# Kernel optimization log

Hardware: AMD Instinct MI355X
Metric: run time of the kernel (lower is better)

## Reference

```python
import jax, jax.numpy as jnp
import numpy as np

HEADS = 20          # 1280 / 64 head_dim, standard SD UNet attention
LORA_SCALE = 1.0    # lora_scale init arg


def setup_inputs() -> dict:
    key = jax.random.key(0)
    ks = jax.random.split(key, 16)
    def w(k, shape, s=0.02):
        return jax.random.normal(k, shape, dtype=jnp.float32) * s
    H, C, R = 1280, 768, 64  # hidden_size, cross_attention_dim, lora_rank
    return {
        "hidden_states": jax.random.normal(ks[0], (16, 4096, H), dtype=jnp.float32),
        "encoder_hidden_states": jax.random.normal(ks[1], (16, 77, C), dtype=jnp.float32),
        # base attention projections (diffusers: q/k/v no bias, to_out has bias)
        "Wq": w(ks[2], (H, H)), "Wk": w(ks[3], (C, H)), "Wv": w(ks[4], (C, H)),
        "Wo": w(ks[5], (H, H)), "bo": jnp.zeros((H,), dtype=jnp.float32),
        # LoRA adapters (down: in->rank, up: rank->out, no bias)
        "q_down": w(ks[6], (H, R)), "q_up": w(ks[7], (R, H)),
        "k_down": w(ks[8], (C, R)), "k_up": w(ks[9], (R, H)),
        "v_down": w(ks[10], (C, R)), "v_up": w(ks[11], (R, H)),
        "o_down": w(ks[12], (H, R)), "o_up": w(ks[13], (R, H)),
    }


def reference(hidden_states, encoder_hidden_states, Wq, Wk, Wv, Wo, bo,
              q_down, q_up, k_down, k_up, v_down, v_up, o_down, o_up):
    b, sq, _ = hidden_states.shape
    # base projections + LoRA low-rank corrections
    q = hidden_states @ Wq + LORA_SCALE * ((hidden_states @ q_down) @ q_up)
    k = encoder_hidden_states @ Wk + LORA_SCALE * ((encoder_hidden_states @ k_down) @ k_up)
    v = encoder_hidden_states @ Wv + LORA_SCALE * ((encoder_hidden_states @ v_down) @ v_up)

    d = q.shape[-1] // HEADS
    def split_heads(x):  # [b, s, h*d] -> [b, h, s, d]
        return x.reshape(x.shape[0], x.shape[1], HEADS, d).transpose(0, 2, 1, 3)
    qh, kh, vh = split_heads(q), split_heads(k), split_heads(v)

    # scaled dot-product attention (no mask, non-causal, dropout=0)
    scale = 1.0 / np.sqrt(d).astype(np.float32)
    scores = jnp.einsum('bhqd,bhkd->bhqk', qh, kh) * scale
    probs = jax.nn.softmax(scores, axis=-1)
    attn_out = jnp.einsum('bhqk,bhkd->bhqd', probs, vh)
    attn_out = attn_out.transpose(0, 2, 1, 3).reshape(b, sq, HEADS * d)

    # output projection + LoRA on W_O
    out = attn_out @ Wo + bo + LORA_SCALE * ((attn_out @ o_down) @ o_up)
    return out
```

## Files before the change

### kernel.cpp

```cpp
#include <hip/hip_runtime.h>
#include <hip/hip_bf16.h>
#include <stdint.h>

typedef unsigned short u16;
typedef __attribute__((ext_vector_type(8))) short short8;
typedef __attribute__((ext_vector_type(4))) float f32x4;

__device__ __forceinline__ u16 f2bf(float f) {
  union { float f; unsigned u; } v; v.f = f;
  unsigned r = v.u + 0x7fffu + ((v.u >> 16) & 1u);
  return (u16)(r >> 16);
}

__device__ __forceinline__ void g2lds16(const u16* g, u16* l) {
  __builtin_amdgcn_global_load_lds(
      (const __attribute__((address_space(1))) uint32_t*)g,
      (__attribute__((address_space(3))) uint32_t*)l, 16, 0, 0);
}

#define BAR()   asm volatile("s_barrier" ::: "memory")
#define LGKM0() asm volatile("s_waitcnt lgkmcnt(0)" ::: "memory")
#define VM8()   asm volatile("s_waitcnt vmcnt(8)" ::: "memory")
#define VM6()   asm volatile("s_waitcnt vmcnt(6)" ::: "memory")
#define VM0()   asm volatile("s_waitcnt vmcnt(0)" ::: "memory")
#define PRIO1() __builtin_amdgcn_s_setprio(1)
#define PRIO0() __builtin_amdgcn_s_setprio(0)

#define QSCALE 0.18033688f

__global__ __launch_bounds__(256) void k_prepc(
    const float* __restrict__ hs, u16* __restrict__ hs_b,
    const float* __restrict__ ehs, u16* __restrict__ ehs_b,
    const float* __restrict__ Wq, const float* __restrict__ qd, const float* __restrict__ qu, u16* __restrict__ wq_t,
    const float* __restrict__ Wk, const float* __restrict__ kd, const float* __restrict__ ku, u16* __restrict__ wk_t,
    const float* __restrict__ Wv, const float* __restrict__ vd, const float* __restrict__ vu, u16* __restrict__ wv_t,
    const float* __restrict__ Wo, const float* __restrict__ od, const float* __restrict__ ou, u16* __restrict__ wo_t) {
  __shared__ float dn[64][65];
  __shared__ float up[64][17];
  int bid = blockIdx.x;

  if (bid < 40960) {
    int i = bid * 256 + threadIdx.x;
    const float4* p = (const float4*)(hs + (size_t)i * 8);
    float4 a = p[0], b = p[1];
    short8 o;
    o[0] = (short)f2bf(a.x); o[1] = (short)f2bf(a.y);
    o[2] = (short)f2bf(a.z); o[3] = (short)f2bf(a.w);
    o[4] = (short)f2bf(b.x); o[5] = (short)f2bf(b.y);
    o[6] = (short)f2bf(b.z); o[7] = (short)f2bf(b.w);
    *(short8*)(hs_b + (size_t)i * 8) = o;
    return;
  }
  bid -= 40960;
  if (bid < 480) {
    int i = bid * 256 + threadIdx.x;
    short8 o;
    if (i < 118272) {
      const float4* p = (const float4*)(ehs + (size_t)i * 8);
      float4 a = p[0], b = p[1];
      o[0] = (short)f2bf(a.x); o[1] = (short)f2bf(a.y);
      o[2] = (short)f2bf(a.z); o[3] = (short)f2bf(a.w);
      o[4] = (short)f2bf(b.x); o[5] = (short)f2bf(b.y);
      o[6] = (short)f2bf(b.z); o[7] = (short)f2bf(b.w);
    } else {
#pragma unroll
      for (int e = 0; e < 8; ++e) o[e] = 0;
    }
    *(short8*)(ehs_b + (size_t)i * 8) = o;
    return;
  }
  bid -= 480;
  const float *W, *dng, *upg; u16* Wt; int K, bx, by;
  if (bid < 1600)      { W = Wq; dng = qd; upg = qu; Wt = wq_t; K = 1280; bx = bid % 20; by = bid / 20; }
  else if (bid < 2560) { bid -= 1600; W = Wk; dng = kd; upg = ku; Wt = wk_t; K = 768;  bx = bid % 12; by = bid / 12; }
  else if (bid < 3520) { bid -= 2560; W = Wv; dng = vd; upg = vu; Wt = wv_t; K = 768;  bx = bid % 12; by = bid / 12; }
  else                 { bid -= 3520; W = Wo; dng = od; upg = ou; Wt = wo_t; K = 1280; bx = bid % 20; by = bid / 20; }
  const int N = 1280;
  const int k0 = bx * 64, n0 = by * 16;
  const int kc = threadIdx.x & 63, ty = threadIdx.x >> 6;
  for (int c = threadIdx.x; c < 4096; c += 256)
    dn[c >> 6][c & 63] = dng[(size_t)(k0 + (c >> 6)) * 64 + (c & 63)];
  for (int c = threadIdx.x; c < 1024; c += 256)
    up[c >> 4][c & 15] = upg[(size_t)(c >> 4) * N + n0 + (c & 15)];
  __syncthreads();
  float acc[4];
#pragma unroll
  for (int e = 0; e < 4; ++e)
    acc[e] = W[(size_t)(k0 + kc) * N + n0 + ty * 4 + e];
#pragma unroll 16
  for (int r = 0; r < 64; ++r) {
    float d = dn[kc][r];
#pragma unroll
    for (int e = 0; e < 4; ++e) acc[e] += d * up[r][ty * 4 + e];
  }
#pragma unroll
  for (int e = 0; e < 4; ++e)
    Wt[(size_t)(n0 + ty * 4 + e) * K + k0 + kc] = f2bf(acc[e]);
}

__global__ __launch_bounds__(256) void k_gemmKV(const u16* __restrict__ A,
                                                const u16* __restrict__ BtK,
                                                const u16* __restrict__ BtV,
                                                u16* __restrict__ CK,
                                                u16* __restrict__ CV) {
  constexpr int N = 1280, K = 768;
  const u16* Bt = blockIdx.z ? BtV : BtK;
  u16* Cout = blockIdx.z ? CV : CK;
  __shared__ __align__(16) u16 As[128 * 32];
  __shared__ __align__(16) u16 Bs[128 * 32];
  const int tid = threadIdx.x, lane = tid & 63, w = tid >> 6;
  const int n0 = blockIdx.x * 128, m0 = blockIdx.y * 128;
  const int wm = (w >> 1) * 64, wn = (w & 1) * 64;

  f32x4 acc[4][4];
  f32x4 zf = {0.f, 0.f, 0.f, 0.f};
#pragma unroll
  for (int i = 0; i < 4; ++i)
#pragma unroll
    for (int j = 0; j < 4; ++j) acc[i][j] = zf;

  const int c0 = w, c1 = w + 4;
  const int rA0 = c0 * 16 + (lane >> 2), rA1 = c1 * 16 + (lane >> 2);
  const int kp = (lane & 3) * 8;
  const u16* gA0 = A + (size_t)(m0 + rA0) * K + kp;
  const u16* gA1 = A + (size_t)(m0 + rA1) * K + kp;
  const u16* gB0 = Bt + (size_t)(n0 + rA0) * K + kp;
  const u16* gB1 = Bt + (size_t)(n0 + rA1) * K + kp;
  u16* lA0 = As + c0 * 512;  u16* lA1 = As + c1 * 512;
  u16* lB0 = Bs + c0 * 512;  u16* lB1 = Bs + c1 * 512;

  const int fr = lane & 15, kg = (lane >> 4) * 8;

  for (int k0 = 0; k0 < K; k0 += 32) {
    g2lds16(gA0 + k0, lA0);
    g2lds16(gA1 + k0, lA1);
    g2lds16(gB0 + k0, lB0);
    g2lds16(gB1 + k0, lB1);
    __syncthreads();
    short8 af[4], bf[4];
#pragma unroll
    for (int i = 0; i < 4; ++i)
      af[i] = *(const short8*)(As + (wm + i * 16 + fr) * 32 + kg);
#pragma unroll
    for (int j = 0; j < 4; ++j)
      bf[j] = *(const short8*)(Bs + (wn + j * 16 + fr) * 32 + kg);
#pragma unroll
    for (int i = 0; i < 4; ++i)
#pragma unroll
      for (int j = 0; j < 4; ++j)
        acc[i][j] = __builtin_amdgcn_mfma_f32_16x16x32_bf16(af[i], bf[j], acc[i][j], 0, 0, 0);
    __syncthreads();
  }

  const int rb = (lane >> 4) * 4;
#pragma unroll
  for (int i = 0; i < 4; ++i)
#pragma unroll
    for (int j = 0; j < 4; ++j) {
      int col = n0 + wn + j * 16 + fr;
#pragma unroll
      for (int r = 0; r < 4; ++r) {
        int row = m0 + wm + i * 16 + rb + r;
        Cout[(size_t)row * N + col] = f2bf(acc[i][j][r]);
      }
    }
}

#define GEMM256_COMMON()                                                       \
  constexpr int K = 1280;                                                      \
  constexpr int N = 1280;                                                      \
  __shared__ __align__(16) u16 lds[2][2][2][128 * 64];                         \
  const int lane = threadIdx.x & 63, w = threadIdx.x >> 6;                     \
  const int bid = blockIdx.x;                                                  \
  const int tile = (bid & 7) * 160 + (bid >> 3);                               \
  const int n0 = (tile % 5) * 256, m0 = (tile / 5) * 256;                      \
  const int l0 = w * 2;                                                        \
  const int fr = lane & 15;                                                    \
  const int q16b = (lane >> 4) * 16;                                           \
  const int xr = (fr & 7) << 4;                                                \
  const int cT0 = ((0 + q16b) ^ xr) >> 1;                                      \
  const int cT1 = ((64 + q16b) ^ xr) >> 1;                                     \
  const int ha = w >> 2;                                                       \
  const int hb = (w & 3) >> 1;                                                 \
  const int rB0 = (w & 1) * 64;

#define GSRC_INIT(A_, Bt_)                                                     \
  const u16* gsrc[4][2];                                                       \
  _Pragma("unroll") for (int s2 = 0; s2 < 4; ++s2) {                           \
    const int side = s2 >> 1, h = s2 & 1;                                      \
    _Pragma("unroll") for (int l = 0; l < 2; ++l) {                            \
      const int o = (l0 + l) * 1024 + lane * 16;                               \
      const int row = o >> 7;                                                  \
      const int scol = (o & 127) ^ ((row & 7) << 4);                           \
      const u16* base = side ? ((Bt_) + (size_t)(n0 + h * 128 + row) * K)      \
                             : ((A_) + (size_t)(m0 + h * 128 + row) * K);      \
      gsrc[s2][l] = base + (scol >> 1);                                        \
    }                                                                          \
  }

#define STAGE_HALF(P, SIDE, H, KT)                                             \
  do {                                                                         \
    g2lds16(gsrc[(SIDE) * 2 + (H)][0] + (KT) * 64,                             \
            &lds[P][SIDE][H][(l0 + 0) * 512]);                                 \
    g2lds16(gsrc[(SIDE) * 2 + (H)][1] + (KT) * 64,                             \
            &lds[P][SIDE][H][(l0 + 1) * 512]);                                 \
  } while (0)

#define STAGE_FULL(P, KT)                                                      \
  do {                                                                         \
    STAGE_HALF(P, 0, 0, KT); STAGE_HALF(P, 0, 1, KT);                          \
    STAGE_HALF(P, 1, 0, KT); STAGE_HALF(P, 1, 1, KT);                          \
  } while (0)

#define LOAD_AF(P, IB)                                                         \
  do {                                                                         \
    _Pragma("unroll") for (int ii = 0; ii < 4; ++ii) {                         \
      const u16* rp = &lds[P][0][ha][(((IB) + ii) * 16 + fr) * 64];            \
      af[ii][0] = *(const short8*)(rp + cT0);                                  \
      af[ii][1] = *(const short8*)(rp + cT1);                                  \
    }                                                                          \
  } while (0)

#define LOAD_BF(P, JB)                                                         \
  do {                                                                         \
    _Pragma("unroll") for (int jj = 0; jj < 2; ++jj) {                         \
      const u16* rp = &lds[P][1][hb][(rB0 + ((JB) + jj) * 16 + fr) * 64];      \
      bf[(JB) + jj][0] = *(const short8*)(rp + cT0);                           \
      bf[(JB) + jj][1] = *(const short8*)(rp + cT1);                           \
    }                                                                          \
  } while (0)

#define MFMA_Q(IO, JB)                                                         \
  do {                                                                         \
    _Pragma("unroll") for (int t = 0; t < 2; ++t)                              \
        _Pragma("unroll") for (int ii = 0; ii < 4; ++ii)                       \
            _Pragma("unroll") for (int jj = 0; jj < 2; ++jj)                   \
                acc[(IO) + ii][(JB) + jj] =                                    \
        __builtin_amdgcn_mfma_f32_16x16x32_bf16(                               \
            af[ii][t], bf[(JB) + jj][t], acc[(IO) + ii][(JB) + jj], 0, 0, 0);  \
  } while (0)

#define ACC_ZERO()                                                             \
  do {                                                                         \
    f32x4 zf = {0.f, 0.f, 0.f, 0.f};                                           \
    _Pragma("unroll") for (int i = 0; i < 8; ++i)                              \
        _Pragma("unroll") for (int j = 0; j < 4; ++j) acc[i][j] = zf;          \
  } while (0)

#define GEMM256_EPI_F32BIAS()                                                  \
  do {                                                                         \
    float* C = (float*)Cout;                                                   \
    _Pragma("unroll") for (int i = 0; i < 8; ++i)                              \
        _Pragma("unroll") for (int j = 0; j < 4; ++j) {                        \
      const int col = ocol + j * 16 + fr;                                      \
      const float bj = bias[col];                                              \
      _Pragma("unroll") for (int r = 0; r < 4; ++r)                            \
          C[(size_t)(orow + i * 16 + rb + r) * N + col] = acc[i][j][r] + bj;   \
    }                                                                          \
  } while (0)

#define GEMM256_EPI_BF16SCALE()                                                \
  do {                                                                         \
    u16* C = (u16*)Cout;                                                       \
    _Pragma("unroll") for (int i = 0; i < 8; ++i)                              \
        _Pragma("unroll") for (int j = 0; j < 4; ++j) {                        \
      const int col = ocol + j * 16 + fr;                                      \
      _Pragma("unroll") for (int r = 0; r < 4; ++r)                            \
          C[(size_t)(orow + i * 16 + rb + r) * N + col] =                      \
              f2bf(acc[i][j][r] * QSCALE);                                     \
    }                                                                          \
  } while (0)

template <int OUT_MODE>
__global__ __launch_bounds__(512, 2) void k_gemm256f(const u16* __restrict__ A,
                                                     const u16* __restrict__ Bt,
                                                     void* __restrict__ Cout,
                                                     const float* __restrict__ bias) {
  GEMM256_COMMON();
  GSRC_INIT(A, Bt);

  short8 af[4][2], bf[4][2];
  f32x4 acc[8][4];
  ACC_ZERO();

  STAGE_FULL(0, 0);
  STAGE_FULL(1, 1);
  VM8();
  BAR();

  for (int t = 0; t < 20; ++t) {
    const int P = t & 1;
    LOAD_AF(P, 0);
    LOAD_BF(P, 0);
    LOAD_BF(P, 2);
    MFMA_Q(0, 0);
    MFMA_Q(0, 2);
    LOAD_AF(P, 4);
    MFMA_Q(4, 2);
    LGKM0();
    BAR();
    if (t < 18) STAGE_FULL(P, t + 2);
    PRIO1(); MFMA_Q(4, 0); PRIO0();
    if (t < 18) { VM8(); } else { VM0(); }
    BAR();
  }

  const int rb = (lane >> 4) * 4;
  const int orow = m0 + (w >> 2) * 128;
  const int ocol = n0 + (w & 3) * 64;
  if (OUT_MODE == 1) { GEMM256_EPI_F32BIAS(); }
  else               { GEMM256_EPI_BF16SCALE(); }
}

__global__ __launch_bounds__(512, 2) void k_gemm256p(const u16* __restrict__ A,
                                                     const u16* __restrict__ Bt,
                                                     void* __restrict__ Cout) {
  GEMM256_COMMON();
  GSRC_INIT(A, Bt);

  short8 af[4][2], bf[4][2];
  f32x4 acc[8][4];
  ACC_ZERO();

  STAGE_FULL(0, 0);
  STAGE_FULL(1, 1);
  VM8();
  BAR();

  for (int it = 0; it < 10; ++it) {
    const bool st = (it < 9);
    const int t2 = 2 * it + 2, t3 = 2 * it + 3;
    LOAD_AF(0, 0); LOAD_BF(0, 0);
    BAR(); LGKM0(); PRIO1(); MFMA_Q(0, 0); PRIO0(); BAR();
    LOAD_BF(0, 2);
    BAR(); LGKM0(); PRIO1(); MFMA_Q(0, 2); PRIO0(); BAR();
    LOAD_AF(0, 4);
    if (st) STAGE_HALF(0, 1, 0, t2);
    BAR(); LGKM0(); PRIO1(); MFMA_Q(4, 2); PRIO0(); BAR();
    if (st) { STAGE_HALF(0, 1, 1, t2); STAGE_HALF(0, 0, 0, t2); }
    PRIO1(); MFMA_Q(4, 0); PRIO0();
    if (st) { VM6(); } else { VM0(); }
    BAR();
    LOAD_AF(1, 0); LOAD_BF(1, 0);
    if (st) STAGE_HALF(0, 0, 1, t2);
    BAR(); LGKM0(); PRIO1(); MFMA_Q(0, 0); PRIO0(); BAR();
    LOAD_BF(1, 2);
    BAR(); LGKM0(); PRIO1(); MFMA_Q(0, 2); PRIO0(); BAR();
    LOAD_AF(1, 4);
    if (st) STAGE_HALF(1, 1, 0, t3);
    BAR(); LGKM0(); PRIO1(); MFMA_Q(4, 2); PRIO0(); BAR();
    if (st) { STAGE_HALF(1, 1, 1, t3); STAGE_HALF(1, 0, 0, t3); STAGE_HALF(1, 0, 1, t3); }
    PRIO1(); MFMA_Q(4, 0); PRIO0();
    if (st) { VM8(); } else { VM0(); }
    BAR();
  }

  const int rb = (lane >> 4) * 4;
  const int orow = m0 + (w >> 2) * 128;
  const int ocol = n0 + (w & 3) * 64;
  GEMM256_EPI_BF16SCALE();
}

__global__ __launch_bounds__(256) void k_attn(u16* __restrict__ Q,
                                              const u16* __restrict__ Kb,
                                              const u16* __restrict__ Vb) {
  const int mt = blockIdx.x, h = blockIdx.y, b = blockIdx.z;
  const int tid = threadIdx.x, lane = tid & 63, w = tid >> 6;
  const int m0 = b * 4096 + mt * 128;
  const int ccol = h * 64;

  __shared__ __align__(16) u16 Qs[128 * 64];
  __shared__ __align__(16) u16 Kl[80 * 72];
  __shared__ __align__(16) u16 Vt[64 * 104];
  __shared__ __align__(16) u16 Pl[128 * 104];

#pragma unroll
  for (int c = 0; c < 4; ++c) {
    const int o = (c * 4 + w) * 1024 + lane * 16;
    const int row = o >> 7;
    const int scol = (o & 127) ^ ((row & 7) << 4);
    g2lds16(Q + (size_t)(m0 + row) * 1280 + ccol + (scol >> 1),
            Qs + (size_t)(c * 4 + w) * 512);
  }

  {
    short8 zz;
#pragma unroll
    for (int e = 0; e < 8; ++e) zz[e] = 0;
    if (tid < 27) ((short8*)Kl)[693 + tid] = zz;
    { const int prow = tid >> 1, pc0 = 80 + (tid & 1) * 8;
      *(short8*)(Pl + prow * 104 + pc0) = zz; }
    for (int c = tid; c < 2048; c += 256)
      Vt[(c >> 5) * 104 + 64 + (c & 31)] = 0;
  }
  for (int c = tid; c < 616; c += 256) {
    int s = c >> 3, d0 = (c & 7) * 8;
    short8 v = *(const short8*)(Kb + (size_t)(b * 77 + s) * 1280 + ccol + d0);
    *(short8*)(Kl + s * 72 + d0) = v;
  }
  for (int c = tid; c < 616; c += 256) {
    int s = c >> 3, d0 = (c & 7) * 8;
    short8 v = *(const short8*)(Vb + (size_t)(b * 77 + s) * 1280 + ccol + d0);
#pragma unroll
    for (int e = 0; e < 8; ++e) Vt[(d0 + e) * 104 + s] = (u16)v[e];
  }
  __syncthreads();

  const int cb = lane & 15;
  const int kq = lane >> 4;
  const int kgu = kq * 8;

  short8 qf[2][2];
#pragma unroll
  for (int i = 0; i < 2; ++i)
#pragma unroll
    for (int t2 = 0; t2 < 2; ++t2) {
      const int r_ = w * 32 + i * 16 + cb;
      const int bc = (t2 * 64 + kq * 16) ^ ((r_ & 7) << 4);
      qf[i][t2] = *(const short8*)(Qs + r_ * 64 + (bc >> 1));
    }

  f32x4 sc[2][5];
  {
    f32x4 zf = {0.f, 0.f, 0.f, 0.f};
#pragma unroll
    for (int i = 0; i < 2; ++i)
#pragma unroll
      for (int j = 0; j < 5; ++j) sc[i][j] = zf;
  }
#pragma unroll
  for (int t2 = 0; t2 < 2; ++t2) {
    short8 kf[5];
#pragma unroll
    for (int j = 0; j < 5; ++j)
      kf[j] = *(const short8*)(Kl + (j * 16 + cb) * 72 + t2 * 32 + kgu);
#pragma unroll
    for (int i = 0; i < 2; ++i)
#pragma unroll
      for (int j = 0; j < 5; ++j)
        sc[i][j] = __builtin_amdgcn_mfma_f32_16x16x32_bf16(qf[i][t2], kf[j], sc[i][j], 0, 0, 0);
  }

  float inv[2][4];
#pragma unroll
  for (int i = 0; i < 2; ++i) {
#pragma unroll
    for (int r = 0; r < 4; ++r) {
      float sum = 0.f;
#pragma unroll
      for (int j = 0; j < 4; ++j) {
        float pv = exp2f(sc[i][j][r]);
        sc[i][j][r] = pv;
        sum += pv;
      }
      {
        float pv = (cb < 13) ? exp2f(sc[i][4][r]) : 0.f;
        sc[i][4][r] = pv;
        sum += pv;
      }
#pragma unroll
      for (int mk = 8; mk >= 1; mk >>= 1) sum += __shfl_xor(sum, mk, 64);
      inv[i][r] = 1.f / sum;
    }
  }

  {
    const int rbase = kq * 4;
#pragma unroll
    for (int i = 0; i < 2; ++i)
#pragma unroll
      for (int j = 0; j < 5; ++j)
#pragma unroll
        for (int r = 0; r < 4; ++r)
          Pl[(w * 32 + i * 16 + rbase + r) * 104 + j * 16 + cb] = f2bf(sc[i][j][r]);
  }
  __syncthreads();

  f32x4 o[2][4];
  {
    f32x4 zf = {0.f, 0.f, 0.f, 0.f};
#pragma unroll
    for (int i = 0; i < 2; ++i)
#pragma unroll
      for (int n = 0; n < 4; ++n) o[i][n] = zf;
  }
#pragma unroll
  for (int t2 = 0; t2 < 3; ++t2) {
    short8 pf[2], vf[4];
#pragma unroll
    for (int i = 0; i < 2; ++i)
      pf[i] = *(const short8*)(Pl + (w * 32 + i * 16 + cb) * 104 + t2 * 32 + kgu);
#pragma unroll
    for (int n = 0; n < 4; ++n)
      vf[n] = *(const short8*)(Vt + (n * 16 + cb) * 104 + t2 * 32 + kgu);
#pragma unroll
    for (int i = 0; i < 2; ++i)
#pragma unroll
      for (int n = 0; n < 4; ++n)
        o[i][n] = __builtin_amdgcn_mfma_f32_16x16x32_bf16(pf[i], vf[n], o[i][n], 0, 0, 0);
  }

  {
    const int rbase = kq * 4;
#pragma unroll
    for (int i = 0; i < 2; ++i)
#pragma unroll
      for (int n = 0; n < 4; ++n)
#pragma unroll
        for (int r = 0; r < 4; ++r)
          Pl[(w * 32 + i * 16 + rbase + r) * 104 + n * 16 + cb] =
              f2bf(o[i][n][r] * inv[i][r]);
  }
  __syncthreads();

#pragma unroll
  for (int c2 = 0; c2 < 4; ++c2) {
    const int o2 = (c2 * 256 + tid) * 16;
    const int row = o2 >> 7, bc = (o2 & 127) >> 1;
    short8 v = *(const short8*)(Pl + row * 104 + bc);
    *(short8*)(Q + (size_t)(m0 + row) * 1280 + ccol + bc) = v;
  }
}

extern "C" void kernel_launch(void* const* d_in, const int* in_sizes, int n_in,
                              void* d_out, int out_size, void* d_ws, size_t ws_size,
                              hipStream_t stream) {
  (void)in_sizes; (void)n_in; (void)out_size; (void)ws_size;
  const float* hs  = (const float*)d_in[0];
  const float* ehs = (const float*)d_in[1];
  const float* Wq  = (const float*)d_in[2];
  const float* Wk  = (const float*)d_in[3];
  const float* Wv  = (const float*)d_in[4];
  const float* Wo  = (const float*)d_in[5];
  const float* bo  = (const float*)d_in[6];
  const float* qd  = (const float*)d_in[7];
  const float* qu  = (const float*)d_in[8];
  const float* kd  = (const float*)d_in[9];
  const float* ku  = (const float*)d_in[10];
  const float* vd  = (const float*)d_in[11];
  const float* vu  = (const float*)d_in[12];
  const float* od  = (const float*)d_in[13];
  const float* ou  = (const float*)d_in[14];

  char* p = (char*)d_ws;
  u16* q_buf = (u16*)p;  p += (size_t)65536 * 1280 * 2;
  u16* wq_t  = (u16*)p;  p += (size_t)1280 * 1280 * 2;
  u16* wo_t  = (u16*)p;  p += (size_t)1280 * 1280 * 2;
  u16* wk_t  = (u16*)p;  p += (size_t)1280 * 768 * 2;
  u16* wv_t  = (u16*)p;  p += (size_t)1280 * 768 * 2;
  u16* ehs_b = (u16*)p;  p += (size_t)1280 * 768 * 2;
  u16* k_buf = (u16*)p;  p += (size_t)1280 * 1280 * 2;
  u16* v_buf = (u16*)p;  p += (size_t)1280 * 1280 * 2;
  u16* hs_b  = (u16*)d_out;

  k_prepc<<<46560, 256, 0, stream>>>(hs, hs_b, ehs, ehs_b,
                                     Wq, qd, qu, wq_t,
                                     Wk, kd, ku, wk_t,
                                     Wv, vd, vu, wv_t,
                                     Wo, od, ou, wo_t);

  k_gemm256p<<<1280, 512, 0, stream>>>(hs_b, wq_t, q_buf);
  k_gemmKV<<<dim3(10, 10, 2), 256, 0, stream>>>(ehs_b, wk_t, wv_t, k_buf, v_buf);

  k_attn<<<dim3(32, 20, 16), 256, 0, stream>>>(q_buf, k_buf, v_buf);

  k_gemm256f<1><<<1280, 512, 0, stream>>>(q_buf, wo_t, d_out, bo);
}
```

Measured before the change: 726.1 us.

## Fuse attention into Q-projection GEMM epilogue with pre-transposed V

Removes the separate attention kernel and computes attention directly in the Q-projection GEMM epilogue. Each wave of a 256x256 tile owns one 64-wide head, loads that head's K and V fragments straight from global memory into registers, and runs softmax(QK)V over 32-row chunks using LDS scratch. The KV GEMM now writes V already transposed per head, padded to 96 keys and zero-filled in the prep kernel, so no LDS transpose is needed. This drops the write and re-read of the Q buffer and one kernel launch. In exchange it runs at one block per CU instead of two and replaces the previous hand-scheduled Q GEMM main loop with the simpler shared one.

Result: faster. 704.7 us, median of 2 (-2.9%).

```diff
diff --git a/kernel.cpp b/kernel.cpp
--- a/kernel.cpp
+++ b/kernel.cpp
@@ -21,7 +21,6 @@
 #define BAR()   asm volatile("s_barrier" ::: "memory")
 #define LGKM0() asm volatile("s_waitcnt lgkmcnt(0)" ::: "memory")
 #define VM8()   asm volatile("s_waitcnt vmcnt(8)" ::: "memory")
-#define VM6()   asm volatile("s_waitcnt vmcnt(6)" ::: "memory")
 #define VM0()   asm volatile("s_waitcnt vmcnt(0)" ::: "memory")
 #define PRIO1() __builtin_amdgcn_s_setprio(1)
 #define PRIO0() __builtin_amdgcn_s_setprio(0)
@@ -31,6 +30,7 @@
 __global__ __launch_bounds__(256) void k_prepc(
     const float* __restrict__ hs, u16* __restrict__ hs_b,
     const float* __restrict__ ehs, u16* __restrict__ ehs_b,
+    u16* __restrict__ vt,
     const float* __restrict__ Wq, const float* __restrict__ qd, const float* __restrict__ qu, u16* __restrict__ wq_t,
     const float* __restrict__ Wk, const float* __restrict__ kd, const float* __restrict__ ku, u16* __restrict__ wk_t,
     const float* __restrict__ Wv, const float* __restrict__ vd, const float* __restrict__ vu, u16* __restrict__ wv_t,
@@ -70,6 +70,15 @@
     return;
   }
   bid -= 480;
+  if (bid < 960) {
+    int i = bid * 256 + threadIdx.x;
+    short8 z;
+#pragma unroll
+    for (int e = 0; e < 8; ++e) z[e] = 0;
+    *(short8*)(vt + (size_t)i * 8) = z;
+    return;
+  }
+  bid -= 960;
   const float *W, *dng, *upg; u16* Wt; int K, bx, by;
   if (bid < 1600)      { W = Wq; dng = qd; upg = qu; Wt = wq_t; K = 1280; bx = bid % 20; by = bid / 20; }
   else if (bid < 2560) { bid -= 1600; W = Wk; dng = kd; upg = ku; Wt = wk_t; K = 768;  bx = bid % 12; by = bid / 12; }
@@ -102,10 +111,9 @@
                                                 const u16* __restrict__ BtK,
                                                 const u16* __restrict__ BtV,
                                                 u16* __restrict__ CK,
-                                                u16* __restrict__ CV) {
+                                                u16* __restrict__ VT) {
   constexpr int N = 1280, K = 768;
   const u16* Bt = blockIdx.z ? BtV : BtK;
-  u16* Cout = blockIdx.z ? CV : CK;
   __shared__ __align__(16) u16 As[128 * 32];
   __shared__ __align__(16) u16 Bs[128 * 32];
   const int tid = threadIdx.x, lane = tid & 63, w = tid >> 6;
@@ -153,17 +161,36 @@
   }
 
   const int rb = (lane >> 4) * 4;
-#pragma unroll
-  for (int i = 0; i < 4; ++i)
-#pragma unroll
-    for (int j = 0; j < 4; ++j) {
-      int col = n0 + wn + j * 16 + fr;
-#pragma unroll
-      for (int r = 0; r < 4; ++r) {
-        int row = m0 + wm + i * 16 + rb + r;
-        Cout[(size_t)row * N + col] = f2bf(acc[i][j][r]);
+  if (blockIdx.z == 0) {
+#pragma unroll
+    for (int i = 0; i < 4; ++i)
+#pragma unroll
+      for (int j = 0; j < 4; ++j) {
+        int col = n0 + wn + j * 16 + fr;
+#pragma unroll
+        for (int r = 0; r < 4; ++r) {
+          int row = m0 + wm + i * 16 + rb + r;
+          CK[(size_t)row * N + col] = f2bf(acc[i][j][r]);
+        }
       }
-    }
+  } else {
+#pragma unroll
+    for (int i = 0; i < 4; ++i)
+#pragma unroll
+      for (int j = 0; j < 4; ++j) {
+        int col = n0 + wn + j * 16 + fr;
+        int h = col >> 6, d = col & 63;
+#pragma unroll
+        for (int r = 0; r < 4; ++r) {
+          int row = m0 + wm + i * 16 + rb + r;
+          if (row < 1232) {
+            int b2 = row / 77;
+            int s2 = row - b2 * 77;
+            VT[(size_t)((b2 * 20 + h) * 64 + d) * 96 + s2] = f2bf(acc[i][j][r]);
+          }
+        }
+      }
+  }
 }
 
 #define GEMM256_COMMON()                                                       \
@@ -247,278 +274,203 @@
         _Pragma("unroll") for (int j = 0; j < 4; ++j) acc[i][j] = zf;          \
   } while (0)
 
-#define GEMM256_EPI_F32BIAS()                                                  \
-  do {                                                                         \
-    float* C = (float*)Cout;                                                   \
-    _Pragma("unroll") for (int i = 0; i < 8; ++i)                              \
-        _Pragma("unroll") for (int j = 0; j < 4; ++j) {                        \
-      const int col = ocol + j * 16 + fr;                                      \
-      const float bj = bias[col];                                              \
-      _Pragma("unroll") for (int r = 0; r < 4; ++r)                            \
-          C[(size_t)(orow + i * 16 + rb + r) * N + col] = acc[i][j][r] + bj;   \
+#define GEMM256_MAINLOOP()                                                     \
+  do {                                                                         \
+    STAGE_FULL(0, 0);                                                          \
+    STAGE_FULL(1, 1);                                                          \
+    VM8();                                                                     \
+    BAR();                                                                     \
+    for (int t = 0; t < 20; ++t) {                                             \
+      const int P = t & 1;                                                     \
+      LOAD_AF(P, 0);                                                           \
+      LOAD_BF(P, 0);                                                           \
+      LOAD_BF(P, 2);                                                           \
+      MFMA_Q(0, 0);                                                            \
+      MFMA_Q(0, 2);                                                            \
+      LOAD_AF(P, 4);                                                           \
+      MFMA_Q(4, 2);                                                            \
+      LGKM0();                                                                 \
+      BAR();                                                                   \
+      if (t < 18) STAGE_FULL(P, t + 2);                                        \
+      PRIO1(); MFMA_Q(4, 0); PRIO0();                                          \
+      if (t < 18) { VM8(); } else { VM0(); }                                   \
+      BAR();                                                                   \
     }                                                                          \
   } while (0)
 
-#define GEMM256_EPI_BF16SCALE()                                                \
-  do {                                                                         \
-    u16* C = (u16*)Cout;                                                       \
-    _Pragma("unroll") for (int i = 0; i < 8; ++i)                              \
-        _Pragma("unroll") for (int j = 0; j < 4; ++j) {                        \
-      const int col = ocol + j * 16 + fr;                                      \
-      _Pragma("unroll") for (int r = 0; r < 4; ++r)                            \
-          C[(size_t)(orow + i * 16 + rb + r) * N + col] =                      \
-              f2bf(acc[i][j][r] * QSCALE);                                     \
-    }                                                                          \
-  } while (0)
-
-template <int OUT_MODE>
 __global__ __launch_bounds__(512, 2) void k_gemm256f(const u16* __restrict__ A,
                                                      const u16* __restrict__ Bt,
-                                                     void* __restrict__ Cout,
+                                                     float* __restrict__ Cout,
                                                      const float* __restrict__ bias) {
   GEMM256_COMMON();
   GSRC_INIT(A, Bt);
-
   short8 af[4][2], bf[4][2];
   f32x4 acc[8][4];
   ACC_ZERO();
-
-  STAGE_FULL(0, 0);
-  STAGE_FULL(1, 1);
-  VM8();
-  BAR();
-
-  for (int t = 0; t < 20; ++t) {
-    const int P = t & 1;
-    LOAD_AF(P, 0);
-    LOAD_BF(P, 0);
-    LOAD_BF(P, 2);
-    MFMA_Q(0, 0);
-    MFMA_Q(0, 2);
-    LOAD_AF(P, 4);
-    MFMA_Q(4, 2);
-    LGKM0();
-    BAR();
-    if (t < 18) STAGE_FULL(P, t + 2);
-    PRIO1(); MFMA_Q(4, 0); PRIO0();
-    if (t < 18) { VM8(); } else { VM0(); }
-    BAR();
-  }
+  GEMM256_MAINLOOP();
 
   const int rb = (lane >> 4) * 4;
   const int orow = m0 + (w >> 2) * 128;
   const int ocol = n0 + (w & 3) * 64;
-  if (OUT_MODE == 1) { GEMM256_EPI_F32BIAS(); }
-  else               { GEMM256_EPI_BF16SCALE(); }
-}
-
-__global__ __launch_bounds__(512, 2) void k_gemm256p(const u16* __restrict__ A,
-                                                     const u16* __restrict__ Bt,
-                                                     void* __restrict__ Cout) {
+#pragma unroll
+  for (int i = 0; i < 8; ++i)
+#pragma unroll
+    for (int j = 0; j < 4; ++j) {
+      const int col = ocol + j * 16 + fr;
+      const float bj = bias[col];
+#pragma unroll
+      for (int r = 0; r < 4; ++r)
+        Cout[(size_t)(orow + i * 16 + rb + r) * N + col] = acc[i][j][r] + bj;
+    }
+}
+
+__global__ __launch_bounds__(512, 1) void k_gemm256qa(const u16* __restrict__ A,
+                                                      const u16* __restrict__ Bt,
+                                                      const u16* __restrict__ Kbuf,
+                                                      const u16* __restrict__ VTg,
+                                                      u16* __restrict__ Obuf) {
   GEMM256_COMMON();
   GSRC_INIT(A, Bt);
-
   short8 af[4][2], bf[4][2];
   f32x4 acc[8][4];
   ACC_ZERO();
-
-  STAGE_FULL(0, 0);
-  STAGE_FULL(1, 1);
-  VM8();
-  BAR();
-
-  for (int it = 0; it < 10; ++it) {
-    const bool st = (it < 9);
-    const int t2 = 2 * it + 2, t3 = 2 * it + 3;
-    LOAD_AF(0, 0); LOAD_BF(0, 0);
-    BAR(); LGKM0(); PRIO1(); MFMA_Q(0, 0); PRIO0(); BAR();
-    LOAD_BF(0, 2);
-    BAR(); LGKM0(); PRIO1(); MFMA_Q(0, 2); PRIO0(); BAR();
-    LOAD_AF(0, 4);
-    if (st) STAGE_HALF(0, 1, 0, t2);
-    BAR(); LGKM0(); PRIO1(); MFMA_Q(4, 2); PRIO0(); BAR();
-    if (st) { STAGE_HALF(0, 1, 1, t2); STAGE_HALF(0, 0, 0, t2); }
-    PRIO1(); MFMA_Q(4, 0); PRIO0();
-    if (st) { VM6(); } else { VM0(); }
-    BAR();
-    LOAD_AF(1, 0); LOAD_BF(1, 0);
-    if (st) STAGE_HALF(0, 0, 1, t2);
-    BAR(); LGKM0(); PRIO1(); MFMA_Q(0, 0); PRIO0(); BAR();
-    LOAD_BF(1, 2);
-    BAR(); LGKM0(); PRIO1(); MFMA_Q(0, 2); PRIO0(); BAR();
-    LOAD_AF(1, 4);
-    if (st) STAGE_HALF(1, 1, 0, t3);
-    BAR(); LGKM0(); PRIO1(); MFMA_Q(4, 2); PRIO0(); BAR();
-    if (st) { STAGE_HALF(1, 1, 1, t3); STAGE_HALF(1, 0, 0, t3); STAGE_HALF(1, 0, 1, t3); }
-    PRIO1(); MFMA_Q(4, 0); PRIO0();
-    if (st) { VM8(); } else { VM0(); }
-    BAR();
-  }
-
-  const int rb = (lane >> 4) * 4;
+  GEMM256_MAINLOOP();
+
+  const int bb = (tile / 5) >> 4;
+  const int hd = (tile % 5) * 4 + (w & 3);
   const int orow = m0 + (w >> 2) * 128;
-  const int ocol = n0 + (w & 3) * 64;
-  GEMM256_EPI_BF16SCALE();
-}
-
-__global__ __launch_bounds__(256) void k_attn(u16* __restrict__ Q,
-                                              const u16* __restrict__ Kb,
-                                              const u16* __restrict__ Vb) {
-  const int mt = blockIdx.x, h = blockIdx.y, b = blockIdx.z;
-  const int tid = threadIdx.x, lane = tid & 63, w = tid >> 6;
-  const int m0 = b * 4096 + mt * 128;
-  const int ccol = h * 64;
-
-  __shared__ __align__(16) u16 Qs[128 * 64];
-  __shared__ __align__(16) u16 Kl[80 * 72];
-  __shared__ __align__(16) u16 Vt[64 * 104];
-  __shared__ __align__(16) u16 Pl[128 * 104];
-
-#pragma unroll
-  for (int c = 0; c < 4; ++c) {
-    const int o = (c * 4 + w) * 1024 + lane * 16;
-    const int row = o >> 7;
-    const int scol = (o & 127) ^ ((row & 7) << 4);
-    g2lds16(Q + (size_t)(m0 + row) * 1280 + ccol + (scol >> 1),
-            Qs + (size_t)(c * 4 + w) * 512);
-  }
+  const int cb = fr, kq = lane >> 4, kgu = kq * 8;
+
+  u16* ldsb = (u16*)lds;
+  u16* Qc = ldsb + w * 2304;
+  u16* Pw = ldsb + 8 * 2304 + w * 3328;
 
   {
     short8 zz;
 #pragma unroll
     for (int e = 0; e < 8; ++e) zz[e] = 0;
-    if (tid < 27) ((short8*)Kl)[693 + tid] = zz;
-    { const int prow = tid >> 1, pc0 = 80 + (tid & 1) * 8;
-      *(short8*)(Pl + prow * 104 + pc0) = zz; }
-    for (int c = tid; c < 2048; c += 256)
-      Vt[(c >> 5) * 104 + 64 + (c & 31)] = 0;
-  }
-  for (int c = tid; c < 616; c += 256) {
-    int s = c >> 3, d0 = (c & 7) * 8;
-    short8 v = *(const short8*)(Kb + (size_t)(b * 77 + s) * 1280 + ccol + d0);
-    *(short8*)(Kl + s * 72 + d0) = v;
-  }
-  for (int c = tid; c < 616; c += 256) {
-    int s = c >> 3, d0 = (c & 7) * 8;
-    short8 v = *(const short8*)(Vb + (size_t)(b * 77 + s) * 1280 + ccol + d0);
-#pragma unroll
-    for (int e = 0; e < 8; ++e) Vt[(d0 + e) * 104 + s] = (u16)v[e];
-  }
-  __syncthreads();
-
-  const int cb = lane & 15;
-  const int kq = lane >> 4;
-  const int kgu = kq * 8;
-
-  short8 qf[2][2];
-#pragma unroll
-  for (int i = 0; i < 2; ++i)
-#pragma unroll
-    for (int t2 = 0; t2 < 2; ++t2) {
-      const int r_ = w * 32 + i * 16 + cb;
-      const int bc = (t2 * 64 + kq * 16) ^ ((r_ & 7) << 4);
-      qf[i][t2] = *(const short8*)(Qs + r_ * 64 + (bc >> 1));
-    }
-
-  f32x4 sc[2][5];
-  {
-    f32x4 zf = {0.f, 0.f, 0.f, 0.f};
-#pragma unroll
-    for (int i = 0; i < 2; ++i)
-#pragma unroll
-      for (int j = 0; j < 5; ++j) sc[i][j] = zf;
-  }
-#pragma unroll
-  for (int t2 = 0; t2 < 2; ++t2) {
-    short8 kf[5];
-#pragma unroll
-    for (int j = 0; j < 5; ++j)
-      kf[j] = *(const short8*)(Kl + (j * 16 + cb) * 72 + t2 * 32 + kgu);
-#pragma unroll
-    for (int i = 0; i < 2; ++i)
+    *(short8*)(Pw + (lane >> 1) * 104 + 80 + (lane & 1) * 8) = zz;
+  }
+
+  short8 kf[5][2];
+#pragma unroll
+  for (int j = 0; j < 5; ++j)
+#pragma unroll
+    for (int t2 = 0; t2 < 2; ++t2)
+      kf[j][t2] = *(const short8*)(Kbuf + (size_t)(bb * 77 + j * 16 + cb) * 1280 +
+                                   hd * 64 + t2 * 32 + kgu);
+  short8 vf[4][3];
+#pragma unroll
+  for (int n = 0; n < 4; ++n)
+#pragma unroll
+    for (int t2 = 0; t2 < 3; ++t2)
+      vf[n][t2] = *(const short8*)(VTg + (size_t)((bb * 20 + hd) * 64 + n * 16 + cb) * 96 +
+                                   t2 * 32 + kgu);
+
+#pragma unroll
+  for (int c = 0; c < 4; ++c) {
+#pragma unroll
+    for (int i2 = 0; i2 < 2; ++i2)
+#pragma unroll
+      for (int j = 0; j < 4; ++j)
+#pragma unroll
+        for (int r = 0; r < 4; ++r)
+          Qc[(i2 * 16 + kq * 4 + r) * 72 + j * 16 + fr] =
+              f2bf(acc[2 * c + i2][j][r] * QSCALE);
+    short8 qf[2][2];
+#pragma unroll
+    for (int i2 = 0; i2 < 2; ++i2)
+#pragma unroll
+      for (int t2 = 0; t2 < 2; ++t2)
+        qf[i2][t2] = *(const short8*)(Qc + (i2 * 16 + cb) * 72 + t2 * 32 + kgu);
+
+    f32x4 sc[2][5];
+    {
+      f32x4 zf = {0.f, 0.f, 0.f, 0.f};
+#pragma unroll
+      for (int i2 = 0; i2 < 2; ++i2)
+#pragma unroll
+        for (int j = 0; j < 5; ++j) sc[i2][j] = zf;
+    }
+#pragma unroll
+    for (int t2 = 0; t2 < 2; ++t2)
+#pragma unroll
+      for (int i2 = 0; i2 < 2; ++i2)
+#pragma unroll
+        for (int j = 0; j < 5; ++j)
+          sc[i2][j] = __builtin_amdgcn_mfma_f32_16x16x32_bf16(
+              qf[i2][t2], kf[j][t2], sc[i2][j], 0, 0, 0);
+
+    float inv[2][4];
+#pragma unroll
+    for (int i2 = 0; i2 < 2; ++i2) {
+#pragma unroll
+      for (int r = 0; r < 4; ++r) {
+        float sum = 0.f;
+#pragma unroll
+        for (int j = 0; j < 4; ++j) {
+          float pv = exp2f(sc[i2][j][r]);
+          sc[i2][j][r] = pv;
+          sum += pv;
+        }
+        {
+          float pv = (cb < 13) ? exp2f(sc[i2][4][r]) : 0.f;
+          sc[i2][4][r] = pv;
+          sum += pv;
+        }
+#pragma unroll
+        for (int mk = 8; mk >= 1; mk >>= 1) sum += __shfl_xor(sum, mk, 64);
+        inv[i2][r] = 1.f / sum;
+      }
+    }
+
+#pragma unroll
+    for (int i2 = 0; i2 < 2; ++i2)
 #pragma unroll
       for (int j = 0; j < 5; ++j)
-        sc[i][j] = __builtin_amdgcn_mfma_f32_16x16x32_bf16(qf[i][t2], kf[j], sc[i][j], 0, 0, 0);
-  }
-
-  float inv[2][4];
-#pragma unroll
-  for (int i = 0; i < 2; ++i) {
-#pragma unroll
-    for (int r = 0; r < 4; ++r) {
-      float sum = 0.f;
-#pragma unroll
-      for (int j = 0; j < 4; ++j) {
-        float pv = exp2f(sc[i][j][r]);
-        sc[i][j][r] = pv;
-        sum += pv;
+#pragma unroll
+        for (int r = 0; r < 4; ++r)
+          Pw[(i2 * 16 + kq * 4 + r) * 104 + j * 16 + cb] = f2bf(sc[i2][j][r]);
+
+    f32x4 o[2][4];
+    {
+      f32x4 zf = {0.f, 0.f, 0.f, 0.f};
+#pragma unroll
+      for (int i2 = 0; i2 < 2; ++i2)
+#pragma unroll
+        for (int n = 0; n < 4; ++n) o[i2][n] = zf;
+    }
+#pragma unroll
+    for (int t2 = 0; t2 < 3; ++t2) {
+      short8 pf[2];
+#pragma unroll
+      for (int i2 = 0; i2 < 2; ++i2)
+        pf[i2] = *(const short8*)(Pw + (i2 * 16 + cb) * 104 + t2 * 32 + kgu);
+#pragma unroll
+      for (int i2 = 0; i2 < 2; ++i2)
+#pragma unroll
+        for (int n = 0; n < 4; ++n)
+          o[i2][n] = __builtin_amdgcn_mfma_f32_16x16x32_bf16(
+              pf[i2], vf[n][t2], o[i2][n], 0, 0, 0);
+    }
+
+#pragma unroll
+    for (int i2 = 0; i2 < 2; ++i2)
+#pragma unroll
+      for (int n = 0; n < 4; ++n)
+#pragma unroll
+        for (int r = 0; r < 4; ++r)
+          Qc[(i2 * 16 + kq * 4 + r) * 72 + n * 16 + cb] =
+              f2bf(o[i2][n][r] * inv[i2][r]);
+    {
+      const int lr2 = lane >> 3, lc2 = (lane & 7) * 8;
+#pragma unroll
+      for (int it = 0; it < 4; ++it) {
+        const int rl = it * 8 + lr2;
+        short8 v = *(const short8*)(Qc + rl * 72 + lc2);
+        *(short8*)(Obuf + (size_t)(orow + c * 32 + rl) * 1280 + hd * 64 + lc2) = v;
       }
-      {
-        float pv = (cb < 13) ? exp2f(sc[i][4][r]) : 0.f;
-        sc[i][4][r] = pv;
-        sum += pv;
-      }
-#pragma unroll
-      for (int mk = 8; mk >= 1; mk >>= 1) sum += __shfl_xor(sum, mk, 64);
-      inv[i][r] = 1.f / sum;
-    }
-  }
-
-  {
-    const int rbase = kq * 4;
-#pragma unroll
-    for (int i = 0; i < 2; ++i)
-#pragma unroll
-      for (int j = 0; j < 5; ++j)
-#pragma unroll
-        for (int r = 0; r < 4; ++r)
-          Pl[(w * 32 + i * 16 + rbase + r) * 104 + j * 16 + cb] = f2bf(sc[i][j][r]);
-  }
-  __syncthreads();
-
-  f32x4 o[2][4];
-  {
-    f32x4 zf = {0.f, 0.f, 0.f, 0.f};
-#pragma unroll
-    for (int i = 0; i < 2; ++i)
-#pragma unroll
-      for (int n = 0; n < 4; ++n) o[i][n] = zf;
-  }
-#pragma unroll
-  for (int t2 = 0; t2 < 3; ++t2) {
-    short8 pf[2], vf[4];
-#pragma unroll
-    for (int i = 0; i < 2; ++i)
-      pf[i] = *(const short8*)(Pl + (w * 32 + i * 16 + cb) * 104 + t2 * 32 + kgu);
-#pragma unroll
-    for (int n = 0; n < 4; ++n)
-      vf[n] = *(const short8*)(Vt + (n * 16 + cb) * 104 + t2 * 32 + kgu);
-#pragma unroll
-    for (int i = 0; i < 2; ++i)
-#pragma unroll
-      for (int n = 0; n < 4; ++n)
-        o[i][n] = __builtin_amdgcn_mfma_f32_16x16x32_bf16(pf[i], vf[n], o[i][n], 0, 0, 0);
-  }
-
-  {
-    const int rbase = kq * 4;
-#pragma unroll
-    for (int i = 0; i < 2; ++i)
-#pragma unroll
-      for (int n = 0; n < 4; ++n)
-#pragma unroll
-        for (int r = 0; r < 4; ++r)
-          Pl[(w * 32 + i * 16 + rbase + r) * 104 + n * 16 + cb] =
-              f2bf(o[i][n][r] * inv[i][r]);
-  }
-  __syncthreads();
-
-#pragma unroll
-  for (int c2 = 0; c2 < 4; ++c2) {
-    const int o2 = (c2 * 256 + tid) * 16;
-    const int row = o2 >> 7, bc = (o2 & 127) >> 1;
-    short8 v = *(const short8*)(Pl + row * 104 + bc);
-    *(short8*)(Q + (size_t)(m0 + row) * 1280 + ccol + bc) = v;
+    }
   }
 }
 
@@ -550,19 +502,18 @@
   u16* wv_t  = (u16*)p;  p += (size_t)1280 * 768 * 2;
   u16* ehs_b = (u16*)p;  p += (size_t)1280 * 768 * 2;
   u16* k_buf = (u16*)p;  p += (size_t)1280 * 1280 * 2;
-  u16* v_buf = (u16*)p;  p += (size_t)1280 * 1280 * 2;
+  u16* vt    = (u16*)p;  p += (size_t)16 * 20 * 64 * 96 * 2;
   u16* hs_b  = (u16*)d_out;
 
-  k_prepc<<<46560, 256, 0, stream>>>(hs, hs_b, ehs, ehs_b,
+  k_prepc<<<47520, 256, 0, stream>>>(hs, hs_b, ehs, ehs_b, vt,
                                      Wq, qd, qu, wq_t,
                                      Wk, kd, ku, wk_t,
                                      Wv, vd, vu, wv_t,
                                      Wo, od, ou, wo_t);
 
-  k_gemm256p<<<1280, 512, 0, stream>>>(hs_b, wq_t, q_buf);
-  k_gemmKV<<<dim3(10, 10, 2), 256, 0, stream>>>(ehs_b, wk_t, wv_t, k_buf, v_buf);
-
-  k_attn<<<dim3(32, 20, 16), 256, 0, stream>>>(q_buf, k_buf, v_buf);
-
-  k_gemm256f<1><<<1280, 512, 0, stream>>>(q_buf, wo_t, d_out, bo);
-}
+  k_gemmKV<<<dim3(10, 10, 2), 256, 0, stream>>>(ehs_b, wk_t, wv_t, k_buf, vt);
+
+  k_gemm256qa<<<1280, 512, 0, stream>>>(hs_b, wq_t, k_buf, vt, q_buf);
+
+  k_gemm256f<<<1280, 512, 0, stream>>>(q_buf, wo_t, (float*)d_out, bo);
+}
```
